# Optimization experiments

Hardware: AMD Instinct MI355X
Metric: run time of the kernel (lower is better)

Reference implementation:

```python
import jax, jax.numpy as jnp
import numpy as np

N_NODES = 100000
N_EDGES = 1250000
D = 64
N_LAYERS = 4


def setup_inputs() -> dict:
    key = jax.random.key(0)
    ks = jax.random.split(key, 6)
    x = jax.random.normal(ks[0], (N_NODES, D), dtype=jnp.float32)
    edge_index = jax.random.randint(ks[1], (2, N_EDGES), 0, N_NODES, dtype=jnp.int64)
    s = 1.0 / np.sqrt(D)
    # PyG SAGEConv per layer: lin_l (applied to aggregated neighbors, with bias)
    # and lin_r (applied to self features, no bias). All layers are 64->64, so stack.
    Wl = jax.random.uniform(ks[2], (N_LAYERS, D, D), dtype=jnp.float32, minval=-s, maxval=s)
    bl = jax.random.uniform(ks[3], (N_LAYERS, D), dtype=jnp.float32, minval=-s, maxval=s)
    Wr = jax.random.uniform(ks[4], (N_LAYERS, D, D), dtype=jnp.float32, minval=-s, maxval=s)
    return {"x": x, "edge_index": edge_index, "Wl": Wl, "bl": bl, "Wr": Wr}


def reference(x, edge_index, Wl, bl, Wr):
    src = edge_index[0]  # message source: x_j
    dst = edge_index[1]  # aggregate at target node
    h = x
    for i in range(N_LAYERS):
        msg = h[src]  # [E, D] irregular gather
        agg = jax.ops.segment_max(msg, dst, num_segments=N_NODES)  # max-pool aggregation
        agg = jnp.where(jnp.isneginf(agg), 0.0, agg)  # empty segments -> 0 (PyG convention)
        h = jax.nn.relu(agg @ Wl[i] + bl[i] + h @ Wr[i])
    return h
```

## Files before the change

### kernel.cpp

```cpp
#include <hip/hip_runtime.h>
#include <hip/hip_fp16.h>
#include <stdint.h>

#define NN 100000
#define NE 1250000
#define DD 64
#define NL 4

#define NPART3 256
#define PSIZE3 391
#define TILE4 1024
#define NTB ((NE / 4 + TILE4 - 1) / TILE4)
#define SCANA_N (NPART3 * NTB)
#define SRCBITS 17

#define MB2 64
#define L2BLOCKS ((NN + MB2 - 1) / MB2)
#define APAD 136
#define CPADH 72
#define CPADF 68

typedef _Float16 half8 __attribute__((ext_vector_type(8)));
typedef _Float16 half2v __attribute__((ext_vector_type(2)));
typedef float floatx4 __attribute__((ext_vector_type(4)));
typedef int intx4 __attribute__((ext_vector_type(4)));

__device__ __forceinline__ unsigned f2h2(float a, float b) {
    __half2 h = __floats2half2_rn(a, b);
    return *reinterpret_cast<unsigned*>(&h);
}
__device__ __forceinline__ unsigned umax2(unsigned a, unsigned b) {
    half2v x = *reinterpret_cast<half2v*>(&a);
    half2v y = *reinterpret_cast<half2v*>(&b);
    half2v r = __builtin_elementwise_max(x, y);
    return *reinterpret_cast<unsigned*>(&r);
}
__device__ __forceinline__ void umax4(uint4& a, uint4 u) {
    a.x = umax2(a.x, u.x); a.y = umax2(a.y, u.y);
    a.z = umax2(a.z, u.z); a.w = umax2(a.w, u.w);
}

__global__ __launch_bounds__(256) void cast_kernel(const float* __restrict__ x,
                                                   __half* __restrict__ hh) {
    int i = blockIdx.x * 256 + threadIdx.x;
    float4 v = ((const float4*)x)[i];
    uint2 u;
    u.x = f2h2(v.x, v.y);
    u.y = f2h2(v.z, v.w);
    ((uint2*)hh)[i] = u;
}

__global__ __launch_bounds__(256) void countA_kernel(const int* __restrict__ dst,
                                                     int* __restrict__ blockcnt) {
    __shared__ int cnt[NPART3];
    int tid = threadIdx.x;
    cnt[tid] = 0;
    __syncthreads();
    int b = blockIdx.x;
    #pragma unroll
    for (int r = 0; r < 4; ++r) {
        int i4 = b * TILE4 + r * 256 + tid;
        if (i4 < NE / 4) {
            intx4 d = __builtin_nontemporal_load(&((const intx4*)dst)[i4]);
            atomicAdd(&cnt[(unsigned)d.x / PSIZE3], 1);
            atomicAdd(&cnt[(unsigned)d.y / PSIZE3], 1);
            atomicAdd(&cnt[(unsigned)d.z / PSIZE3], 1);
            atomicAdd(&cnt[(unsigned)d.w / PSIZE3], 1);
        }
    }
    __syncthreads();
    blockcnt[tid * NTB + b] = cnt[tid];
}

__global__ __launch_bounds__(512) void scanP1_kernel(int* __restrict__ blockcnt,
                                                     int* __restrict__ rowsum) {
    __shared__ int sm[512];
    int p = blockIdx.x;
    int tid = threadIdx.x;
    int v = (tid < NTB) ? blockcnt[p * NTB + tid] : 0;
    sm[tid] = v;
    __syncthreads();
    for (int off = 1; off < 512; off <<= 1) {
        int t = (tid >= off) ? sm[tid - off] : 0;
        __syncthreads();
        sm[tid] += t;
        __syncthreads();
    }
    if (tid < NTB) blockcnt[p * NTB + tid] = sm[tid] - v;
    if (tid == 511) rowsum[p] = sm[511];
}

__global__ __launch_bounds__(256) void scanP2_kernel(int* __restrict__ rowsum) {
    __shared__ int sm[256];
    int tid = threadIdx.x;
    int v = rowsum[tid];
    sm[tid] = v;
    __syncthreads();
    for (int off = 1; off < 256; off <<= 1) {
        int t = (tid >= off) ? sm[tid - off] : 0;
        __syncthreads();
        sm[tid] += t;
        __syncthreads();
    }
    rowsum[tid] = sm[tid] - v;
}

__global__ __launch_bounds__(256) void scatterA_kernel(const int* __restrict__ src,
                                                       const int* __restrict__ dst,
                                                       const int* __restrict__ blockcnt,
                                                       const int* __restrict__ rowoff,
                                                       int* __restrict__ ebufP) {
    __shared__ int cur[NPART3];
    int tid = threadIdx.x;
    int b = blockIdx.x;
    cur[tid] = rowoff[tid] + blockcnt[tid * NTB + b];
    __syncthreads();
    #pragma unroll
    for (int r = 0; r < 4; ++r) {
        int i4 = b * TILE4 + r * 256 + tid;
        if (i4 < NE / 4) {
            intx4 d = __builtin_nontemporal_load(&((const intx4*)dst)[i4]);
            intx4 s = __builtin_nontemporal_load(&((const intx4*)src)[i4]);
            int part, p;
            part = (unsigned)d.x / PSIZE3; p = atomicAdd(&cur[part], 1);
            ebufP[p] = ((d.x - part * PSIZE3) << SRCBITS) | s.x;
            part = (unsigned)d.y / PSIZE3; p = atomicAdd(&cur[part], 1);
            ebufP[p] = ((d.y - part * PSIZE3) << SRCBITS) | s.y;
            part = (unsigned)d.z / PSIZE3; p = atomicAdd(&cur[part], 1);
            ebufP[p] = ((d.z - part * PSIZE3) << SRCBITS) | s.z;
            part = (unsigned)d.w / PSIZE3; p = atomicAdd(&cur[part], 1);
            ebufP[p] = ((d.w - part * PSIZE3) << SRCBITS) | s.w;
        }
    }
}

__global__ __launch_bounds__(1024) void fillD_kernel(const int* __restrict__ ebufP,
                                                     const int* __restrict__ rowoff,
                                                     int* __restrict__ row_start,
                                                     int* __restrict__ csr) {
    __shared__ int cnt[PSIZE3];
    __shared__ int localstart[PSIZE3];
    __shared__ int partial[1024];
    int part = blockIdx.x;
    int tid = threadIdx.x;
    int nbase = part * PSIZE3;
    int base = rowoff[part];
    int hi = (part < NPART3 - 1) ? rowoff[part + 1] : NE;

    if (tid < PSIZE3) cnt[tid] = 0;
    __syncthreads();

    for (int i = base + tid; i < hi; i += 1024)
        atomicAdd(&cnt[(unsigned)ebufP[i] >> SRCBITS], 1);
    __syncthreads();

    int e0 = (tid < PSIZE3) ? cnt[tid] : 0;
    int s = e0;
    partial[tid] = s;
    __syncthreads();
    for (int off = 1; off < 1024; off <<= 1) {
        int v = (tid >= off) ? partial[tid - off] : 0;
        __syncthreads();
        partial[tid] += v;
        __syncthreads();
    }
    int run = partial[tid] - s;
    if (tid < PSIZE3) localstart[tid] = run;
    __syncthreads();

    int nmax = NN - nbase; if (nmax > PSIZE3) nmax = PSIZE3;
    if (tid < nmax) row_start[nbase + tid] = base + localstart[tid];
    if (part == NPART3 - 1 && tid == 0) row_start[NN] = NE;

    if (tid < PSIZE3) cnt[tid] = 0;
    __syncthreads();

    for (int i = base + tid; i < hi; i += 1024) {
        int p = ebufP[i];
        int dl = (unsigned)p >> SRCBITS;
        int local = atomicAdd(&cnt[dl], 1);
        csr[base + localstart[dl] + local] = p & ((1 << SRCBITS) - 1);
    }
}

__global__ __launch_bounds__(256, 6) void agg_kernel(const __half* __restrict__ hh,
                                                     const int* __restrict__ row_start,
                                                     const int* __restrict__ csr,
                                                     __half* __restrict__ aggh) {
    int tid = threadIdx.x;
    int wv = tid >> 6;
    int lane = tid & 63;
    int nl = lane >> 3;
    int l8 = lane & 7;
    int c8 = l8 * 8;
    int nb = blockIdx.x * 32 + wv * 8;

    int rsl = row_start[nb + ((lane < 9) ? lane : 8)];
    int base = __shfl(rsl, nl, 64);
    int cnt  = __shfl(rsl, nl + 1, 64) - base;
    int cl   = max(cnt - 1, 0);
    int bclamp = min(base, NE - 1);

    int km = cnt;
    km = max(km, __shfl_xor(km, 8, 64));
    km = max(km, __shfl_xor(km, 16, 64));
    km = max(km, __shfl_xor(km, 32, 64));

    const uint4 NI4 = make_uint4(0xFC00FC00u, 0xFC00FC00u, 0xFC00FC00u, 0xFC00FC00u);
    uint4 acc = NI4;
    int lsrc = lane & 56;

    int idx = csr[bclamp + min(l8, cl)];
    for (int k0 = 0; k0 < km; k0 += 8) {
        int nidx = csr[bclamp + min(k0 + 8 + l8, cl)];
        #pragma unroll
        for (int j = 0; j < 8; ++j) {
            int srcv = __shfl(idx, lsrc + j, 64);
            uint4 u = *(const uint4*)&hh[(unsigned)srcv * DD + c8];
            umax4(acc, u);
        }
        idx = nidx;
    }

    if (cnt <= 0) acc = make_uint4(0, 0, 0, 0);
    *(uint4*)&aggh[(size_t)(nb + nl) * DD + c8] = acc;
}

__global__ __launch_bounds__(256, 4) void layer_mfma_kernel(
        const __half* __restrict__ aggh,
        __half* __restrict__ hh,
        float* __restrict__ hout,
        const float* __restrict__ Wl,
        const float* __restrict__ bl,
        const float* __restrict__ Wr,
        int last) {
    __shared__ char smem[2 * MB2 * APAD * 2];
    _Float16* a_s  = (_Float16*)smem;
    _Float16* bt_s = (_Float16*)(smem + MB2 * APAD * 2);

    int tid = threadIdx.x;
    int lane = tid & 63;
    int w = tid >> 6;
    int node0 = blockIdx.x * MB2;

    #pragma unroll
    for (int i = 0; i < 4; ++i) {
        int idx = i * 256 + tid;
        int r = idx >> 4;
        int c4 = idx & 15;
        int node = node0 + r; if (node > NN - 1) node = NN - 1;
        const __half* srcp = (c4 < 8) ? (aggh + (size_t)node * DD + c4 * 8)
                                      : (hh + (size_t)node * DD + (c4 - 8) * 8);
        uint4 v = *(const uint4*)srcp;
        *(uint4*)&a_s[r * APAD + c4 * 8] = v;
    }
    {
        int n = tid & 63;
        int kb = tid >> 6;
        #pragma unroll
        for (int kk = 0; kk < 32; ++kk) {
            int k = kb * 32 + kk;
            float wv = (k < 64) ? Wl[k * DD + n] : Wr[(k - 64) * DD + n];
            bt_s[n * APAD + k] = (_Float16)wv;
        }
    }
    __syncthreads();

    floatx4 acc[4];
    #pragma unroll
    for (int nt = 0; nt < 4; ++nt) acc[nt] = (floatx4){0.f, 0.f, 0.f, 0.f};
    int m = lane & 15;
    int q = lane >> 4;

    #pragma unroll
    for (int ks = 0; ks < 4; ++ks) {
        half8 af = *(half8*)&a_s[(w * 16 + m) * APAD + q * 8 + ks * 32];
        #pragma unroll
        for (int nt = 0; nt < 4; ++nt) {
            half8 bf = *(half8*)&bt_s[(nt * 16 + m) * APAD + q * 8 + ks * 32];
            acc[nt] = __builtin_amdgcn_mfma_f32_16x16x32_f16(af, bf, acc[nt], 0, 0, 0);
        }
    }
    __syncthreads();

    _Float16* ch = (_Float16*)smem;
    float*    cf = (float*)(smem + MB2 * CPADH * 2);

    #pragma unroll
    for (int nt = 0; nt < 4; ++nt) {
        int col = nt * 16 + m;
        float b = bl[col];
        #pragma unroll
        for (int r = 0; r < 4; ++r) {
            int rowl = w * 16 + q * 4 + r;
            float o = fmaxf(acc[nt][r] + b, 0.0f);
            if (last) cf[rowl * CPADF + col] = o;
            else      ch[rowl * CPADH + col] = (_Float16)o;
        }
    }
    __syncthreads();

    if (!last) {
        #pragma unroll
        for (int i = 0; i < 2; ++i) {
            int idx = i * 256 + tid;
            int r = idx >> 3;
            int c4 = idx & 7;
            int node = node0 + r;
            if (node < NN) {
                uint4 v = *(uint4*)&ch[r * CPADH + c4 * 8];
                *(uint4*)&hh[(size_t)node * DD + c4 * 8] = v;
            }
        }
    } else {
        #pragma unroll
        for (int i = 0; i < 4; ++i) {
            int idx = i * 256 + tid;
            int r = idx >> 4;
            int c4 = idx & 15;
            int node = node0 + r;
            if (node < NN) {
                float4 v = *(float4*)&cf[r * CPADF + c4 * 4];
                *(float4*)&hout[(size_t)node * DD + c4 * 4] = v;
            }
        }
    }
}

extern "C" void kernel_launch(void* const* d_in, const int* in_sizes, int n_in,
                              void* d_out, int out_size, void* d_ws, size_t ws_size,
                              hipStream_t stream) {
    const float* x  = (const float*)d_in[0];
    const int*   ei = (const int*)d_in[1];
    const float* Wl = (const float*)d_in[2];
    const float* bl = (const float*)d_in[3];
    const float* Wr = (const float*)d_in[4];
    float* h = (float*)d_out;

    const int* src = ei;
    const int* dst = ei + NE;

    char* ws = (char*)d_ws;
    __half* aggh     = (__half*)ws;  ws += (size_t)NN * DD * sizeof(__half);
    __half* hh       = (__half*)ws;  ws += (size_t)NN * DD * sizeof(__half);
    int* row_start   = (int*)ws;     ws += (size_t)(NN + 16) * sizeof(int);
    int* blockcnt    = (int*)ws;     ws += (size_t)(SCANA_N + 16) * sizeof(int);
    int* rowsum      = (int*)ws;     ws += (size_t)(NPART3 + 16) * sizeof(int);
    int* csr         = (int*)ws;

    int* ebufP = (int*)aggh;

    cast_kernel<<<(NN * DD / 4) / 256, 256, 0, stream>>>(x, hh);

    countA_kernel<<<NTB, 256, 0, stream>>>(dst, blockcnt);
    scanP1_kernel<<<NPART3, 512, 0, stream>>>(blockcnt, rowsum);
    scanP2_kernel<<<1, 256, 0, stream>>>(rowsum);
    scatterA_kernel<<<NTB, 256, 0, stream>>>(src, dst, blockcnt, rowsum, ebufP);
    fillD_kernel<<<NPART3, 1024, 0, stream>>>(ebufP, rowsum, row_start, csr);

    for (int l = 0; l < NL; ++l) {
        agg_kernel<<<NN / 32, 256, 0, stream>>>(hh, row_start, csr, aggh);
        layer_mfma_kernel<<<L2BLOCKS, 256, 0, stream>>>(
            aggh, hh, h, Wl + (size_t)l * DD * DD, bl + (size_t)l * DD, Wr + (size_t)l * DD * DD,
            (l == NL - 1) ? 1 : 0);
    }
}
```

Baseline: 256.6 us.

## Sort nodes by degree class to balance warp work in aggregation

Builds a degree-bucketed node ordering (a histogram in fillD, a class scan, and a scatter into an order array) so that each wavefront's 8 nodes have similar neighbor counts. The aggregation loop runs to the max degree across the 8 nodes, so grouping nodes of similar degree cuts wasted iterations from divergence. In exchange it adds two small preprocessing kernels, one extra indirection per node, and scattered output writes and row_start reads.

```diff
diff --git a/kernel.cpp b/kernel.cpp
--- a/kernel.cpp
+++ b/kernel.cpp
@@ -13,6 +13,7 @@
 #define NTB ((NE / 4 + TILE4 - 1) / TILE4)
 #define SCANA_N (NPART3 * NTB)
 #define SRCBITS 17
+#define NCLS 64
 
 #define MB2 64
 #define L2BLOCKS ((NN + MB2 - 1) / MB2)
@@ -90,9 +91,11 @@
     if (tid == 511) rowsum[p] = sm[511];
 }
 
-__global__ __launch_bounds__(256) void scanP2_kernel(int* __restrict__ rowsum) {
+__global__ __launch_bounds__(256) void scanP2_kernel(int* __restrict__ rowsum,
+                                                     int* __restrict__ clsCnt) {
     __shared__ int sm[256];
     int tid = threadIdx.x;
+    if (tid < NCLS) clsCnt[tid] = 0;
     int v = rowsum[tid];
     sm[tid] = v;
     __syncthreads();
@@ -137,10 +140,12 @@
 __global__ __launch_bounds__(1024) void fillD_kernel(const int* __restrict__ ebufP,
                                                      const int* __restrict__ rowoff,
                                                      int* __restrict__ row_start,
-                                                     int* __restrict__ csr) {
+                                                     int* __restrict__ csr,
+                                                     int* __restrict__ clsCnt) {
     __shared__ int cnt[PSIZE3];
     __shared__ int localstart[PSIZE3];
     __shared__ int partial[1024];
+    __shared__ int clsh[NCLS];
     int part = blockIdx.x;
     int tid = threadIdx.x;
     int nbase = part * PSIZE3;
@@ -148,13 +153,19 @@
     int hi = (part < NPART3 - 1) ? rowoff[part + 1] : NE;
 
     if (tid < PSIZE3) cnt[tid] = 0;
+    if (tid >= 1024 - NCLS) clsh[tid - (1024 - NCLS)] = 0;
     __syncthreads();
 
     for (int i = base + tid; i < hi; i += 1024)
         atomicAdd(&cnt[(unsigned)ebufP[i] >> SRCBITS], 1);
     __syncthreads();
 
+    int nmax = NN - nbase; if (nmax > PSIZE3) nmax = PSIZE3;
     int e0 = (tid < PSIZE3) ? cnt[tid] : 0;
+    if (tid < nmax) {
+        int cls = min((e0 + 7) >> 3, NCLS - 1);
+        atomicAdd(&clsh[cls], 1);
+    }
     int s = e0;
     partial[tid] = s;
     __syncthreads();
@@ -168,7 +179,6 @@
     if (tid < PSIZE3) localstart[tid] = run;
     __syncthreads();
 
-    int nmax = NN - nbase; if (nmax > PSIZE3) nmax = PSIZE3;
     if (tid < nmax) row_start[nbase + tid] = base + localstart[tid];
     if (part == NPART3 - 1 && tid == 0) row_start[NN] = NE;
 
@@ -181,11 +191,47 @@
         int local = atomicAdd(&cnt[dl], 1);
         csr[base + localstart[dl] + local] = p & ((1 << SRCBITS) - 1);
     }
+    if (tid < NCLS && clsh[tid]) atomicAdd(&clsCnt[tid], clsh[tid]);
+}
+
+__global__ __launch_bounds__(64) void clsScan_kernel(const int* __restrict__ clsCnt,
+                                                     int* __restrict__ clsCur) {
+    int tid = threadIdx.x;
+    int v = clsCnt[tid];
+    int s = v;
+    #pragma unroll
+    for (int off = 1; off < 64; off <<= 1) {
+        int t = __shfl(s, (tid >= off) ? (tid - off) : 0, 64);
+        if (tid >= off) s += t;
+    }
+    clsCur[tid] = s - v;
+}
+
+__global__ __launch_bounds__(1024) void clsScatter_kernel(const int* __restrict__ row_start,
+                                                          int* __restrict__ clsCur,
+                                                          int* __restrict__ order) {
+    __shared__ int h[NCLS];
+    __shared__ int basec[NCLS];
+    int tid = threadIdx.x;
+    if (tid < NCLS) h[tid] = 0;
+    __syncthreads();
+    int n = blockIdx.x * 1024 + tid;
+    int cls = 0, rank = 0;
+    if (n < NN) {
+        int c = row_start[n + 1] - row_start[n];
+        cls = min((c + 7) >> 3, NCLS - 1);
+        rank = atomicAdd(&h[cls], 1);
+    }
+    __syncthreads();
+    if (tid < NCLS) basec[tid] = h[tid] ? atomicAdd(&clsCur[tid], h[tid]) : 0;
+    __syncthreads();
+    if (n < NN) order[basec[cls] + rank] = n;
 }
 
 __global__ __launch_bounds__(256, 6) void agg_kernel(const __half* __restrict__ hh,
                                                      const int* __restrict__ row_start,
                                                      const int* __restrict__ csr,
+                                                     const int* __restrict__ order,
                                                      __half* __restrict__ aggh) {
     int tid = threadIdx.x;
     int wv = tid >> 6;
@@ -195,9 +241,11 @@
     int c8 = l8 * 8;
     int nb = blockIdx.x * 32 + wv * 8;
 
-    int rsl = row_start[nb + ((lane < 9) ? lane : 8)];
-    int base = __shfl(rsl, nl, 64);
-    int cnt  = __shfl(rsl, nl + 1, 64) - base;
+    int ord = order[nb + nl];
+    int rs = row_start[ord + (l8 & 1)];
+    int lsrc = lane & 56;
+    int base = __shfl(rs, lsrc, 64);
+    int cnt  = __shfl(rs, lsrc + 1, 64) - base;
     int cl   = max(cnt - 1, 0);
     int bclamp = min(base, NE - 1);
 
@@ -208,7 +256,6 @@
 
     const uint4 NI4 = make_uint4(0xFC00FC00u, 0xFC00FC00u, 0xFC00FC00u, 0xFC00FC00u);
     uint4 acc = NI4;
-    int lsrc = lane & 56;
 
     int idx = csr[bclamp + min(l8, cl)];
     for (int k0 = 0; k0 < km; k0 += 8) {
@@ -223,7 +270,7 @@
     }
 
     if (cnt <= 0) acc = make_uint4(0, 0, 0, 0);
-    *(uint4*)&aggh[(size_t)(nb + nl) * DD + c8] = acc;
+    *(uint4*)&aggh[(size_t)ord * DD + c8] = acc;
 }
 
 __global__ __launch_bounds__(256, 4) void layer_mfma_kernel(
@@ -346,6 +393,9 @@
     int* row_start   = (int*)ws;     ws += (size_t)(NN + 16) * sizeof(int);
     int* blockcnt    = (int*)ws;     ws += (size_t)(SCANA_N + 16) * sizeof(int);
     int* rowsum      = (int*)ws;     ws += (size_t)(NPART3 + 16) * sizeof(int);
+    int* order       = (int*)ws;     ws += (size_t)(NN + 16) * sizeof(int);
+    int* clsCnt      = (int*)ws;     ws += (size_t)(NCLS + 16) * sizeof(int);
+    int* clsCur      = (int*)ws;     ws += (size_t)(NCLS + 16) * sizeof(int);
     int* csr         = (int*)ws;
 
     int* ebufP = (int*)aggh;
@@ -354,12 +404,14 @@
 
     countA_kernel<<<NTB, 256, 0, stream>>>(dst, blockcnt);
     scanP1_kernel<<<NPART3, 512, 0, stream>>>(blockcnt, rowsum);
-    scanP2_kernel<<<1, 256, 0, stream>>>(rowsum);
+    scanP2_kernel<<<1, 256, 0, stream>>>(rowsum, clsCnt);
     scatterA_kernel<<<NTB, 256, 0, stream>>>(src, dst, blockcnt, rowsum, ebufP);
-    fillD_kernel<<<NPART3, 1024, 0, stream>>>(ebufP, rowsum, row_start, csr);
+    fillD_kernel<<<NPART3, 1024, 0, stream>>>(ebufP, rowsum, row_start, csr, clsCnt);
+    clsScan_kernel<<<1, 64, 0, stream>>>(clsCnt, clsCur);
+    clsScatter_kernel<<<(NN + 1023) / 1024, 1024, 0, stream>>>(row_start, clsCur, order);
 
     for (int l = 0; l < NL; ++l) {
-        agg_kernel<<<NN / 32, 256, 0, stream>>>(hh, row_start, csr, aggh);
+        agg_kernel<<<NN / 32, 256, 0, stream>>>(hh, row_start, csr, order, aggh);
         layer_mfma_kernel<<<L2BLOCKS, 256, 0, stream>>>(
             aggh, hh, h, Wl + (size_t)l * DD * DD, bl + (size_t)l * DD, Wr + (size_t)l * DD * DD,
             (l == NL - 1) ? 1 : 0);
```

Result: slower. 268.3 us (+4.5%).
